# Optimization experiments

Hardware: AMD Instinct MI355X
Metric: run time of the kernel (lower is better)

## Reference

```python
import jax, jax.numpy as jnp
import numpy as np
import math

ALGEBRA_DIM = 32

def _hadamard(n):
    H = np.array([[1.0]], dtype=np.float32)
    while H.shape[0] < n:
        H = np.block([[H, H], [H, -H]])
    return H

# Sylvester-ordered Hadamard matrix, normalized: equals the butterfly FHT with /sqrt(N)
H32 = jnp.asarray(_hadamard(ALGEBRA_DIM) / math.sqrt(ALGEBRA_DIM), dtype=jnp.float32)

def quantize_ternary(w):
    # BitNet-b1.58 style absmean ternary quantization with straight-through estimator
    scale = jnp.mean(jnp.abs(w)) + 1e-8
    w_q = jnp.clip(jnp.round(w / scale), -1.0, 1.0) * scale
    return w + jax.lax.stop_gradient(w_q - w)

def setup_inputs() -> dict:
    key = jax.random.key(0)
    k1, k2, k3 = jax.random.split(key, 3)
    B, T = 4, 2048
    in_o = out_o = 128  # in_features = out_features = 4096
    x = jax.random.normal(k1, (B, T, ALGEBRA_DIM * in_o), dtype=jnp.float32)
    weight = jax.random.uniform(k2, (ALGEBRA_DIM, out_o, in_o), dtype=jnp.float32) * 2.0 - 1.0
    alpha = jnp.ones((ALGEBRA_DIM, in_o), dtype=jnp.float32)
    beta_init = math.sqrt(3.0 / (2.0 * in_o))
    beta = jnp.ones((ALGEBRA_DIM, out_o), dtype=jnp.float32) * beta_init
    return {"x": x, "weight": weight, "alpha": alpha, "beta": beta}

def reference(x, weight, alpha, beta):
    B, T, D = x.shape
    G = ALGEBRA_DIM
    in_o = D // G
    w_q = quantize_ternary(weight)                      # [G, out_o, in_o]
    xp = x.reshape(B, T, G, in_o) * alpha               # [B,T,G,in_o]
    # FHT over algebra dim G (Sylvester WHT, /sqrt(G) folded into H32)
    xm = jnp.einsum('btgi,gh->bthi', xp, H32)           # [B,T,G,in_o]
    # grouped ternary matmul: btgi,gio->btgo with w_q transposed
    yp = jnp.einsum('bthi,hoi->btho', xm, w_q)          # [B,T,G,out_o]
    ym = jnp.einsum('btho,hg->btgo', yp, H32)           # FHT over algebra dim again
    y = ym * beta                                       # [B,T,G,out_o]
    return y.reshape(B, T, -1)
```

## Files before the change

### kernel.cpp

```cpp
#include <hip/hip_runtime.h>
#include <cstdint>
#include <cstddef>

#define TM 16
#define IP 136
#define SLAB (TM * IP)

__device__ __forceinline__ unsigned short f2bf(float f) {
  union { float f; unsigned int u; } c; c.f = f;
  unsigned int u = c.u;
  return (unsigned short)((u + 0x7FFFu + ((u >> 16) & 1u)) >> 16);
}
__device__ __forceinline__ float bf2f(unsigned short h) {
  union { unsigned int u; float f; } c; c.u = ((unsigned int)h) << 16; return c.f;
}

__device__ __forceinline__ void fht32(float* v) {
  #pragma unroll
  for (int s = 1; s < 32; s <<= 1) {
    #pragma unroll
    for (int a = 0; a < 32; ++a) {
      if ((a & s) == 0) {
        float u0 = v[a], u1 = v[a + s];
        v[a] = u0 + u1;
        v[a + s] = u0 - u1;
      }
    }
  }
}

typedef __attribute__((ext_vector_type(8))) short bf16x8;
typedef __attribute__((ext_vector_type(4))) float f32x4;

__global__ void kred1(const float* __restrict__ w, double* __restrict__ partials) {
  const int tid = threadIdx.x;
  const int base = blockIdx.x * 1024 + tid;
  double s = 0.0;
  #pragma unroll
  for (int j = 0; j < 4; ++j) s += (double)fabsf(w[base + j * 256]);
  #pragma unroll
  for (int off = 32; off > 0; off >>= 1) s += __shfl_down(s, off, 64);
  __shared__ double sh[4];
  if ((tid & 63) == 0) sh[tid >> 6] = s;
  __syncthreads();
  if (tid == 0) partials[blockIdx.x] = sh[0] + sh[1] + sh[2] + sh[3];
}

__global__ void kred2(const double* __restrict__ partials,
                      const float* __restrict__ beta,
                      float* __restrict__ scale_out, float* __restrict__ coef) {
  __shared__ double sh[8];
  __shared__ float s_scale;
  const int tid = threadIdx.x;
  double s = partials[tid];
  #pragma unroll
  for (int off = 32; off > 0; off >>= 1) s += __shfl_down(s, off, 64);
  if ((tid & 63) == 0) sh[tid >> 6] = s;
  __syncthreads();
  if (tid == 0) {
    double t = 0.0;
    #pragma unroll
    for (int k = 0; k < 8; ++k) t += sh[k];
    float sc = (float)(t / 524288.0) + 1e-8f;
    s_scale = sc;
    scale_out[0] = sc;
  }
  __syncthreads();
  const float sc = s_scale;
  for (int c = tid; c < 4096; c += 512)
    coef[c] = beta[c] * sc * (1.0f / 32.0f);
}

__global__ void kquant(const float* __restrict__ w,
                       const float* __restrict__ scale_p,
                       unsigned short* __restrict__ wq) {
  const float sc = scale_p[0];
  const int base = blockIdx.x * 1024 + threadIdx.x;
  #pragma unroll
  for (int j = 0; j < 4; ++j) {
    const int k = base + j * 256;
    float q = rintf(w[k] / sc);
    q = fminf(1.f, fmaxf(-1.f, q));
    wq[k] = f2bf(q);
  }
}

__global__ __launch_bounds__(512, 1) void had_main(
    const float* __restrict__ x,
    const unsigned short* __restrict__ wq,
    const float* __restrict__ alpha,
    const float* __restrict__ coef,
    float* __restrict__ y) {
  extern __shared__ unsigned short lds[];
  const int tid = threadIdx.x;
  const long tok0 = (long)blockIdx.x * TM;
  const int i0 = tid & 127;
  const int tq = tid >> 7;

  {
    float av[32];
    #pragma unroll
    for (int g = 0; g < 32; ++g) av[g] = alpha[g * 128 + i0];
    for (int p = 0; p < 4; ++p) {
      const int t = p * 4 + tq;
      const float* xrow = x + (size_t)(tok0 + t) * 4096 + i0;
      float v[32];
      #pragma unroll
      for (int g = 0; g < 32; ++g) v[g] = xrow[(size_t)g * 128] * av[g];
      fht32(v);
      #pragma unroll
      for (int h = 0; h < 32; ++h) lds[(h * TM + t) * IP + i0] = f2bf(v[h]);
    }
  }
  __syncthreads();

  {
    const int wave = tid >> 6;
    const int lane = tid & 63;
    const int m = lane & 15;
    const int quad = lane >> 4;
    for (int hh = 0; hh < 4; ++hh) {
      const int h = wave + hh * 8;
      unsigned short* slab = lds + h * SLAB;
      bf16x8 afr[4];
      #pragma unroll
      for (int ks = 0; ks < 4; ++ks)
        afr[ks] = *(const bf16x8*)(slab + m * IP + ks * 32 + quad * 8);
      const unsigned short* wh = wq + h * 16384 + quad * 8;
      #pragma unroll
      for (int nt = 0; nt < 8; ++nt) {
        f32x4 acc = {0.f, 0.f, 0.f, 0.f};
        const unsigned short* wb = wh + (nt * 16 + m) * 128;
        #pragma unroll
        for (int ks = 0; ks < 4; ++ks) {
          bf16x8 bfr = *(const bf16x8*)(wb + ks * 32);
          acc = __builtin_amdgcn_mfma_f32_16x16x32_bf16(afr[ks], bfr, acc, 0, 0, 0);
        }
        #pragma unroll
        for (int r = 0; r < 4; ++r)
          slab[(quad * 4 + r) * IP + nt * 16 + m] = f2bf(acc[r]);
      }
    }
  }
  __syncthreads();

  {
    float cf[32];
    #pragma unroll
    for (int g = 0; g < 32; ++g) cf[g] = coef[g * 128 + i0];
    for (int p = 0; p < 4; ++p) {
      const int t = p * 4 + tq;
      float v[32];
      #pragma unroll
      for (int h = 0; h < 32; ++h) v[h] = bf2f(lds[(h * TM + t) * IP + i0]);
      fht32(v);
      float* yrow = y + (size_t)(tok0 + t) * 4096 + i0;
      #pragma unroll
      for (int g = 0; g < 32; ++g) yrow[(size_t)g * 128] = v[g] * cf[g];
    }
  }
}

extern "C" void kernel_launch(void* const* d_in, const int* in_sizes, int n_in,
                              void* d_out, int out_size, void* d_ws, size_t ws_size,
                              hipStream_t stream) {
  (void)in_sizes; (void)n_in; (void)out_size; (void)ws_size;
  const float* x     = (const float*)d_in[0];
  const float* w     = (const float*)d_in[1];
  const float* alpha = (const float*)d_in[2];
  const float* beta  = (const float*)d_in[3];
  float* y = (float*)d_out;

  char* ws = (char*)d_ws;
  unsigned short* wq = (unsigned short*)(ws);
  float* coef      = (float*)(ws + 1048576);
  float* scale     = (float*)(ws + 1064960);
  double* partials = (double*)(ws + 1065472);

  (void)hipFuncSetAttribute(reinterpret_cast<const void*>(had_main),
                            hipFuncAttributeMaxDynamicSharedMemorySize, 139264);

  hipLaunchKernelGGL(kred1,    dim3(512), dim3(256), 0,      stream, w, partials);
  hipLaunchKernelGGL(kred2,    dim3(1),   dim3(512), 0,      stream, partials, beta, scale, coef);
  hipLaunchKernelGGL(kquant,   dim3(512), dim3(256), 0,      stream, w, scale, wq);
  hipLaunchKernelGGL(had_main, dim3(512), dim3(512), 139264, stream, x, wq, alpha, coef, y);
}
```

Before: 305.1 us.

## Halve token tile, pre-swizzle ternary weights into MFMA fragment order, merge prep kernels

The main kernel's token tile drops from 16 to 8, which halves LDS per block and doubles the grid. The launch bound is raised to allow several blocks per CU so memory latency can overlap. Quantized weights are now written in MFMA B-fragment order, so each lane loads its fragment with one contiguous vector read, and the scale and quantize steps are fused into one kernel that replaces kred2 and kquant. The coefficient array is gone: beta times scale is computed inside the main kernel. Half of each MFMA's rows are wasted because only 8 tokens fill the 16-row tile, and the launch bound may limit registers for the 32-element FHT arrays.

Result: faster. 279.3 us (-8.5%).

```diff
diff --git a/kernel.cpp b/kernel.cpp
--- a/kernel.cpp
+++ b/kernel.cpp
@@ -2,7 +2,7 @@
 #include <cstdint>
 #include <cstddef>
 
-#define TM 16
+#define TM 8
 #define IP 136
 #define SLAB (TM * IP)
 
@@ -34,10 +34,10 @@
 
 __global__ void kred1(const float* __restrict__ w, double* __restrict__ partials) {
   const int tid = threadIdx.x;
-  const int base = blockIdx.x * 1024 + tid;
+  const int base = blockIdx.x * 8192 + tid;
   double s = 0.0;
   #pragma unroll
-  for (int j = 0; j < 4; ++j) s += (double)fabsf(w[base + j * 256]);
+  for (int j = 0; j < 32; ++j) s += (double)fabsf(w[base + j * 256]);
   #pragma unroll
   for (int off = 32; off > 0; off >>= 1) s += __shfl_down(s, off, 64);
   __shared__ double sh[4];
@@ -46,50 +46,39 @@
   if (tid == 0) partials[blockIdx.x] = sh[0] + sh[1] + sh[2] + sh[3];
 }
 
-__global__ void kred2(const double* __restrict__ partials,
-                      const float* __restrict__ beta,
-                      float* __restrict__ scale_out, float* __restrict__ coef) {
-  __shared__ double sh[8];
-  __shared__ float s_scale;
+__global__ void kprep(const float* __restrict__ w, const double* __restrict__ partials,
+                      float* __restrict__ scale_out, unsigned short* __restrict__ wqt) {
   const int tid = threadIdx.x;
-  double s = partials[tid];
-  #pragma unroll
-  for (int off = 32; off > 0; off >>= 1) s += __shfl_down(s, off, 64);
-  if ((tid & 63) == 0) sh[tid >> 6] = s;
-  __syncthreads();
-  if (tid == 0) {
-    double t = 0.0;
+  __shared__ float s_sc;
+  if (tid < 64) {
+    double s = partials[tid];
     #pragma unroll
-    for (int k = 0; k < 8; ++k) t += sh[k];
-    float sc = (float)(t / 524288.0) + 1e-8f;
-    s_scale = sc;
-    scale_out[0] = sc;
+    for (int off = 32; off > 0; off >>= 1) s += __shfl_down(s, off, 64);
+    if (tid == 0) s_sc = (float)(s / 524288.0) + 1e-8f;
   }
   __syncthreads();
-  const float sc = s_scale;
-  for (int c = tid; c < 4096; c += 512)
-    coef[c] = beta[c] * sc * (1.0f / 32.0f);
+  const float sc = s_sc;
+  if (blockIdx.x == 0 && tid == 0) scale_out[0] = sc;
+  const int cid = blockIdx.x * 256 + tid;
+  const int lane = cid & 63, ks = (cid >> 6) & 3, nt = (cid >> 8) & 7, h = cid >> 11;
+  const int m = lane & 15, quad = lane >> 4;
+  const float* src = w + h * 16384 + (nt * 16 + m) * 128 + ks * 32 + quad * 8;
+  bf16x8 vv;
+  #pragma unroll
+  for (int j = 0; j < 8; ++j) {
+    float q = rintf(src[j] / sc);
+    q = fminf(1.f, fmaxf(-1.f, q));
+    vv[j] = (short)f2bf(q);
+  }
+  *(bf16x8*)(wqt + (size_t)cid * 8) = vv;
 }
 
-__global__ void kquant(const float* __restrict__ w,
-                       const float* __restrict__ scale_p,
-                       unsigned short* __restrict__ wq) {
-  const float sc = scale_p[0];
-  const int base = blockIdx.x * 1024 + threadIdx.x;
-  #pragma unroll
-  for (int j = 0; j < 4; ++j) {
-    const int k = base + j * 256;
-    float q = rintf(w[k] / sc);
-    q = fminf(1.f, fmaxf(-1.f, q));
-    wq[k] = f2bf(q);
-  }
-}
-
-__global__ __launch_bounds__(512, 1) void had_main(
+__global__ __launch_bounds__(512, 4) void had_main(
     const float* __restrict__ x,
-    const unsigned short* __restrict__ wq,
+    const unsigned short* __restrict__ wqt,
     const float* __restrict__ alpha,
-    const float* __restrict__ coef,
+    const float* __restrict__ beta,
+    const float* __restrict__ scale_p,
     float* __restrict__ y) {
   extern __shared__ unsigned short lds[];
   const int tid = threadIdx.x;
@@ -101,7 +90,8 @@
     float av[32];
     #pragma unroll
     for (int g = 0; g < 32; ++g) av[g] = alpha[g * 128 + i0];
-    for (int p = 0; p < 4; ++p) {
+    #pragma unroll
+    for (int p = 0; p < 2; ++p) {
       const int t = p * 4 + tq;
       const float* xrow = x + (size_t)(tok0 + t) * 4096 + i0;
       float v[32];
@@ -125,30 +115,33 @@
       bf16x8 afr[4];
       #pragma unroll
       for (int ks = 0; ks < 4; ++ks)
-        afr[ks] = *(const bf16x8*)(slab + m * IP + ks * 32 + quad * 8);
-      const unsigned short* wh = wq + h * 16384 + quad * 8;
+        afr[ks] = *(const bf16x8*)(slab + (m & 7) * IP + ks * 32 + quad * 8);
+      const unsigned short* wh = wqt + ((size_t)h * 8) * 2048;
       #pragma unroll
       for (int nt = 0; nt < 8; ++nt) {
         f32x4 acc = {0.f, 0.f, 0.f, 0.f};
-        const unsigned short* wb = wh + (nt * 16 + m) * 128;
         #pragma unroll
         for (int ks = 0; ks < 4; ++ks) {
-          bf16x8 bfr = *(const bf16x8*)(wb + ks * 32);
+          bf16x8 bfr = *(const bf16x8*)(wh + (size_t)(nt * 4 + ks) * 512 + lane * 8);
           acc = __builtin_amdgcn_mfma_f32_16x16x32_bf16(afr[ks], bfr, acc, 0, 0, 0);
         }
-        #pragma unroll
-        for (int r = 0; r < 4; ++r)
-          slab[(quad * 4 + r) * IP + nt * 16 + m] = f2bf(acc[r]);
+        if (quad < 2) {
+          #pragma unroll
+          for (int r = 0; r < 4; ++r)
+            slab[(quad * 4 + r) * IP + nt * 16 + m] = f2bf(acc[r]);
+        }
       }
     }
   }
   __syncthreads();
 
   {
+    const float sc32 = scale_p[0] * (1.0f / 32.0f);
     float cf[32];
     #pragma unroll
-    for (int g = 0; g < 32; ++g) cf[g] = coef[g * 128 + i0];
-    for (int p = 0; p < 4; ++p) {
+    for (int g = 0; g < 32; ++g) cf[g] = beta[g * 128 + i0] * sc32;
+    #pragma unroll
+    for (int p = 0; p < 2; ++p) {
       const int t = p * 4 + tq;
       float v[32];
       #pragma unroll
@@ -172,16 +165,14 @@
   float* y = (float*)d_out;
 
   char* ws = (char*)d_ws;
-  unsigned short* wq = (unsigned short*)(ws);
-  float* coef      = (float*)(ws + 1048576);
-  float* scale     = (float*)(ws + 1064960);
-  double* partials = (double*)(ws + 1065472);
+  unsigned short* wqt = (unsigned short*)(ws);
+  float* scale     = (float*)(ws + 1048576);
+  double* partials = (double*)(ws + 1048584);
 
   (void)hipFuncSetAttribute(reinterpret_cast<const void*>(had_main),
-                            hipFuncAttributeMaxDynamicSharedMemorySize, 139264);
+                            hipFuncAttributeMaxDynamicSharedMemorySize, 69632);
 
-  hipLaunchKernelGGL(kred1,    dim3(512), dim3(256), 0,      stream, w, partials);
-  hipLaunchKernelGGL(kred2,    dim3(1),   dim3(512), 0,      stream, partials, beta, scale, coef);
-  hipLaunchKernelGGL(kquant,   dim3(512), dim3(256), 0,      stream, w, scale, wq);
-  hipLaunchKernelGGL(had_main, dim3(512), dim3(512), 139264, stream, x, wq, alpha, coef, y);
+  hipLaunchKernelGGL(kred1,    dim3(64),   dim3(256), 0,     stream, w, partials);
+  hipLaunchKernelGGL(kprep,    dim3(256),  dim3(256), 0,     stream, w, partials, scale, wqt);
+  hipLaunchKernelGGL(had_main, dim3(1024), dim3(512), 69632, stream, x, wqt, alpha, beta, scale, y);
 }
```
